# Kernel tuning notes

Measured on AMD Instinct MI355X. Metric: run time of the kernel, lower is better.

Reference implementation:

```python
import jax, jax.numpy as jnp
import numpy as np

N_GRAPH = 10000
IN_DIM = 256
HID = 256
N_NODES = 16
FEAT_DIM = 64
N_EDGES = 5
TAU = 0.01


def _gat(x, src, dst, W, al, ar, R, b, H, D, N):
    # DGL GATConv: fc -> per-head attention logits -> edge softmax over dst -> aggregate, residual fc, bias
    h = (x @ W).reshape(N, H, D)                      # [N,H,D]
    el = jnp.sum(h * al[None], -1)                    # [N,H]
    er = jnp.sum(h * ar[None], -1)                    # [N,H]
    e = jax.nn.leaky_relu(el[src] + er[dst], 0.2)     # [E,H]
    m = jax.ops.segment_max(e, dst, num_segments=N)
    ex = jnp.exp(e - m[dst])
    s = jax.ops.segment_sum(ex, dst, num_segments=N)
    alpha = ex / s[dst]                               # [E,H]
    out = jax.ops.segment_sum(alpha[:, :, None] * h[src], dst, num_segments=N)  # [N,H,D]
    out = out + (x @ R).reshape(N, H, D) + b.reshape(1, H, D)
    return out.reshape(N, H * D)


def _masked_softmax(vec, mask, eps=1e-8):
    m = mask.astype(vec.dtype)
    _vec = vec * m - 10000.0 * (1.0 - m)
    vmax = jnp.max(_vec, axis=-1, keepdims=True)
    exps = jnp.exp((vec - vmax) * m) * m
    return exps / (jnp.sum(exps, -1, keepdims=True) + eps)


def _sample_edges(probs, target_idx):
    n, T = probs.shape
    mask = jnp.arange(T) == target_idx                # [T] bool, one-hot of target
    edges = [jnp.full((n,), target_idx, dtype=jnp.int32)]
    key = jax.random.key(42)
    for i in range(N_EDGES - 1):
        p = _masked_softmax(probs, jnp.logical_not(mask))
        idx = jax.random.categorical(jax.random.fold_in(key, i),
                                     jnp.log(jnp.maximum(p, 1e-30)), axis=-1)  # [n]
        mask = jnp.logical_or(jax.nn.one_hot(idx, T, dtype=bool), mask)
        edges.append(idx.astype(jnp.int32))
    return jnp.stack(edges, axis=-1)                  # [n, N_EDGES]


def _forward(feat, W1a, al1a, ar1a, R1a, b1a, W1e, al1e, ar1e, R1e, b1e,
             W2a, al2a, ar2a, R2a, b2a, W2e, al2e, ar2e, R2e, b2e,
             Wt, bt, Wo, bo, src, dst, target_idx):
    N = feat.shape[0]
    tf = jax.nn.leaky_relu(feat[target_idx] @ Wt + bt, 0.01)            # [2*HID]
    a = _gat(feat, src, dst, W1a, al1a, ar1a, R1a, b1a, 4, HID // 4, N)  # [N,HID]
    e = _gat(feat, src, dst, W1e, al1e, ar1e, R1e, b1e, 4, HID // 4, N)  # [N,HID]
    a2 = jax.nn.leaky_relu(jnp.concatenate([a, e], -1) + tf, 0.01)       # [N,2*HID]
    e2 = jax.nn.leaky_relu(jnp.concatenate([e, a], -1) + tf, 0.01)
    a3 = _gat(a2, src, dst, W2a, al2a, ar2a, R2a, b2a, 4, N_NODES * FEAT_DIM // 4, N)  # [N, n_nodes*feat_dim]
    e3 = _gat(e2, src, dst, W2e, al2e, ar2e, R2e, b2e, 1, N_NODES, N)                  # [N, n_nodes]
    attr = a3.reshape(N, N_NODES, FEAT_DIM).mean(0)                     # [n_nodes, feat_dim]
    node_attr = jax.nn.leaky_relu(attr, 0.01) @ Wo + bo                 # [n_nodes, input_dim]
    probs = jax.nn.softmax(e3.T, axis=-1)                               # [n_nodes, N]
    return node_attr, probs


def setup_inputs() -> dict:
    key = jax.random.key(0)
    ks = jax.random.split(key, 32)
    N, IN, H = N_GRAPH, IN_DIM, 4
    E0 = 80000
    feat = jax.random.normal(ks[0], (N, IN), jnp.float32)
    loop = jnp.arange(N, dtype=jnp.int32)
    src = jnp.concatenate([jax.random.randint(ks[1], (E0,), 0, N, jnp.int32), loop])
    dst = jnp.concatenate([jax.random.randint(ks[2], (E0,), 0, N, jnp.int32), loop])

    def p(k, shape, fan):
        return jax.random.normal(k, shape, jnp.float32) * (1.0 / np.sqrt(fan))

    D1 = HID // 4
    D2a = N_NODES * FEAT_DIM // 4
    O2a = N_NODES * FEAT_DIM
    inp = dict(feat=feat, src=src, dst=dst, target_idx=7)
    # layer-1 attr / edge GATs
    inp.update(W1a=p(ks[3], (IN, HID), IN), al1a=p(ks[4], (H, D1), D1), ar1a=p(ks[5], (H, D1), D1),
               R1a=p(ks[6], (IN, HID), IN), b1a=p(ks[7], (HID,), HID))
    inp.update(W1e=p(ks[8], (IN, HID), IN), al1e=p(ks[9], (H, D1), D1), ar1e=p(ks[10], (H, D1), D1),
               R1e=p(ks[11], (IN, HID), IN), b1e=p(ks[12], (HID,), HID))
    # layer-2 attr GAT (4 heads) and edge GAT (1 head)
    inp.update(W2a=p(ks[13], (2 * HID, O2a), 2 * HID), al2a=p(ks[14], (H, D2a), D2a), ar2a=p(ks[15], (H, D2a), D2a),
               R2a=p(ks[16], (2 * HID, O2a), 2 * HID), b2a=p(ks[17], (O2a,), O2a))
    inp.update(W2e=p(ks[18], (2 * HID, N_NODES), 2 * HID), al2e=p(ks[19], (1, N_NODES), N_NODES),
               ar2e=p(ks[20], (1, N_NODES), N_NODES), R2e=p(ks[21], (2 * HID, N_NODES), 2 * HID),
               b2e=p(ks[22], (N_NODES,), N_NODES))
    # target feat layer and attr output layer
    inp.update(Wt=p(ks[23], (IN, 2 * HID), IN), bt=p(ks[24], (2 * HID,), 2 * HID),
               Wo=p(ks[25], (FEAT_DIM, IN), FEAT_DIM), bo=p(ks[26], (IN,), IN))
    return inp


def reference(feat, W1a, al1a, ar1a, R1a, b1a, W1e, al1e, ar1e, R1e, b1e,
              W2a, al2a, ar2a, R2a, b2a, W2e, al2e, ar2e, R2e, b2e,
              Wt, bt, Wo, bo, src, dst, target_idx):
    node_attr, probs = _forward(feat, W1a, al1a, ar1a, R1a, b1a, W1e, al1e, ar1e, R1e, b1e,
                                W2a, al2a, ar2a, R2a, b2a, W2e, al2e, ar2e, R2e, b2e,
                                Wt, bt, Wo, bo, src, dst, target_idx)
    node_edges = _sample_edges(probs, target_idx)
    # (node_attr, attr_sample_weights, node_edges, normalized_edge_sample_weights)
    return node_attr, node_attr, node_edges, probs
```

## Files before the change

kernel.cpp:

```cpp
#include <hip/hip_runtime.h>
#include <hip/hip_bf16.h>

#define NGR 10000
typedef unsigned int u32;
typedef __attribute__((ext_vector_type(8))) short short8;
typedef __attribute__((ext_vector_type(4))) float f32x4;

__device__ __forceinline__ void threefry(u32 k0, u32 k1, u32 c0, u32 c1, u32& o0, u32& o1) {
    u32 ks2 = k0 ^ k1 ^ 0x1BD11BDAu;
    u32 x0 = c0 + k0, x1 = c1 + k1;
#define TF_R(r) { x0 += x1; x1 = (x1 << r) | (x1 >> (32 - r)); x1 ^= x0; }
    TF_R(13) TF_R(15) TF_R(26) TF_R(6)
    x0 += k1; x1 += ks2 + 1u;
    TF_R(17) TF_R(29) TF_R(16) TF_R(24)
    x0 += ks2; x1 += k0 + 2u;
    TF_R(13) TF_R(15) TF_R(26) TF_R(6)
    x0 += k0; x1 += k1 + 3u;
    TF_R(17) TF_R(29) TF_R(16) TF_R(24)
    x0 += k1; x1 += ks2 + 4u;
    TF_R(13) TF_R(15) TF_R(26) TF_R(6)
    x0 += ks2; x1 += k0 + 5u;
#undef TF_R
    o0 = x0; o1 = x1;
}

__global__ void k_deg(const int* __restrict__ dst, int* __restrict__ deg, int E) {
    int i = blockIdx.x * blockDim.x + threadIdx.x;
    if (i < E) atomicAdd(&deg[dst[i]], 1);
}
__global__ void k_scan(const int* __restrict__ deg, int* __restrict__ rowptr, int n) {
    __shared__ int sums[256];
    __shared__ int excl[257];
    const int T = 256;
    int t = threadIdx.x;
    int per = (n + T - 1) / T;
    int lo = t * per, hi = min(lo + per, n);
    int s = 0;
    for (int i = lo; i < hi; ++i) s += deg[i];
    sums[t] = s;
    __syncthreads();
    if (t == 0) { int run = 0; for (int i = 0; i < T; ++i) { excl[i] = run; run += sums[i]; } excl[T] = run; }
    __syncthreads();
    int run = excl[t];
    for (int i = lo; i < hi; ++i) { rowptr[i] = run; run += deg[i]; }
    if (t == 0) rowptr[n] = excl[T];
}
__global__ void k_scatter(const int* __restrict__ dst, const int* __restrict__ rowptr,
                          int* __restrict__ cursor, int* __restrict__ colidx, int E) {
    int i = blockIdx.x * blockDim.x + threadIdx.x;
    if (i >= E) return;
    int d = dst[i];
    int pos = atomicAdd(&cursor[d], 1);
    colidx[rowptr[d] + pos] = i;
}

#define TINYF 1.17549435e-38f
__global__ __launch_bounds__(256) void k_prep(
    const float* __restrict__ feat, const int* __restrict__ tptr,
    const float* __restrict__ Wt, const float* __restrict__ bt,
    const float* __restrict__ W1a, const float* __restrict__ W1e,
    const float* __restrict__ R1a, const float* __restrict__ R1e,
    const float* __restrict__ b1a, const float* __restrict__ b1e,
    const float* __restrict__ W2a, const float* __restrict__ al2a, const float* __restrict__ ar2a,
    unsigned short* __restrict__ feathi, unsigned short* __restrict__ featlo,
    unsigned short* __restrict__ WThi, unsigned short* __restrict__ WTlo,
    float* __restrict__ tf, float* __restrict__ gum, float* __restrict__ wal,
    float* __restrict__ packb, float* __restrict__ zreg)
{
    __shared__ float sh[32 * 33];
    int b = blockIdx.x, tid = threadIdx.x;
    if (b < 2500) {
        int idx = b * 256 + tid;
        float4 v = ((const float4*)feat)[idx];
        ushort4 h, l;
        __hip_bfloat16 bb; float r;
        bb = __float2bfloat16(v.x); h.x = *(unsigned short*)&bb; r = v.x - __bfloat162float(bb);
        bb = __float2bfloat16(r);   l.x = *(unsigned short*)&bb;
        bb = __float2bfloat16(v.y); h.y = *(unsigned short*)&bb; r = v.y - __bfloat162float(bb);
        bb = __float2bfloat16(r);   l.y = *(unsigned short*)&bb;
        bb = __float2bfloat16(v.z); h.z = *(unsigned short*)&bb; r = v.z - __bfloat162float(bb);
        bb = __float2bfloat16(r);   l.z = *(unsigned short*)&bb;
        bb = __float2bfloat16(v.w); h.w = *(unsigned short*)&bb; r = v.w - __bfloat162float(bb);
        bb = __float2bfloat16(r);   l.w = *(unsigned short*)&bb;
        ((ushort4*)feathi)[idx] = h;
        ((ushort4*)featlo)[idx] = l;
        return;
    }
    b -= 2500;
    if (b < 256) {
        int bx = b >> 3, by = b & 7;
        int tx = tid & 31, ty = tid >> 5;
#pragma unroll
        for (int i = ty; i < 32; i += 8) {
            int k = by * 32 + i, c = bx * 32 + tx;
            float v;
            if (c < 256) v = W1a[k * 256 + c];
            else if (c < 512) v = W1e[k * 256 + c - 256];
            else if (c < 768) v = R1a[k * 256 + c - 512];
            else v = R1e[k * 256 + c - 768];
            sh[i * 33 + tx] = v;
        }
        __syncthreads();
#pragma unroll
        for (int i = ty; i < 32; i += 8) {
            float x = sh[tx * 33 + i];
            __hip_bfloat16 bh = __float2bfloat16(x);
            float r = x - __bfloat162float(bh);
            __hip_bfloat16 bl = __float2bfloat16(r);
            WThi[(size_t)(bx * 32 + i) * 256 + by * 32 + tx] = *(unsigned short*)&bh;
            WTlo[(size_t)(bx * 32 + i) * 256 + by * 32 + tx] = *(unsigned short*)&bl;
        }
        return;
    }
    b -= 256;
    if (b < 8) {
        float* frow = sh;
        float* red = sh + 256;
        int t = *tptr;
        frow[tid] = feat[t * 256 + tid];
        __syncthreads();
        int j = b * 64 + (tid & 63);
        int ks = (tid >> 6) * 64;
        float s = 0.f;
#pragma unroll 16
        for (int k = ks; k < ks + 64; ++k) s = fmaf(frow[k], Wt[(size_t)k * 512 + j], s);
        red[tid] = s;
        __syncthreads();
        if (tid < 64) {
            float v = red[tid] + red[tid + 64] + red[tid + 128] + red[tid + 192] + bt[j];
            tf[j] = v >= 0.f ? v : 0.01f * v;
        }
        return;
    }
    b -= 8;
    if (b < 2500) {
        int idx = b * 256 + tid;
        int it = idx / (16 * NGR);
        int f = idx - it * (16 * NGR);
        u32 fk0, fk1, o0, o1;
        threefry(0u, 42u, 0u, (u32)it, fk0, fk1);
        threefry(fk0, fk1, 0u, (u32)f, o0, o1);
        u32 bits = o0 ^ o1;
        float fl = __uint_as_float((bits >> 9) | 0x3F800000u) - 1.0f;
        float u = fmaxf(TINYF, fl + TINYF);
        gum[idx] = -logf(-logf(u));
        return;
    }
    b -= 2500;
    if (b < 16) {
        int o = b * 256 + tid;
        int k = o >> 3, q = o & 7, sel = q >> 2, hh = q & 3;
        const float* av = (sel ? ar2a : al2a) + hh * 256;
        const float* wr = W2a + (size_t)k * 1024 + hh * 256;
        float s = 0.f;
        for (int d = 0; d < 256; ++d) s = fmaf(wr[d], av[d], s);
        wal[k * 8 + q] = s;
        return;
    }
    b -= 16;
    if (b < 235) {
        int idx = b * 256 + tid;
        if (idx < NGR * 6) zreg[idx] = 0.f;
        return;
    }
    b -= 235;
    {
        int c = b * 256 + tid;
        packb[c] = (c < 512) ? 0.f : ((c < 768) ? b1a[c - 512] : b1e[c - 768]);
    }
}

__global__ __launch_bounds__(256) void gemm_bf16x3(
    const unsigned short* __restrict__ Ahi, const unsigned short* __restrict__ Alo,
    const unsigned short* __restrict__ Bhi, const unsigned short* __restrict__ Blo,
    float* __restrict__ C, const float* __restrict__ bias, int M)
{
    constexpr int K = 256;
    __shared__ unsigned short AsH[2][128 * 32];
    __shared__ unsigned short AsL[2][128 * 32];
    __shared__ unsigned short BsH[2][128 * 32];
    __shared__ unsigned short BsL[2][128 * 32];
    const int tid = threadIdx.x;
    const int lane = tid & 63;
    const int w = tid >> 6, wr = w >> 1, wc = w & 1;
    const int bm = blockIdx.y * 128, bn = blockIdx.x * 128;
    const int fr = lane & 15, fq = lane >> 4;
    const int srow = tid >> 2;
    const int sbyte = (tid & 3) * 16;
    f32x4 acc[4][4] = {};

    auto stage = [&](int b, int k0) {
        const char* pA[2] = {(const char*)Ahi, (const char*)Alo};
        const char* pB[2] = {(const char*)Bhi, (const char*)Blo};
        char* dA[2] = {(char*)AsH[b], (char*)AsL[b]};
        char* dB[2] = {(char*)BsH[b], (char*)BsL[b]};
#pragma unroll
        for (int q = 0; q < 2; ++q) {
            const char* ga0 = pA[q] + ((size_t)(bm + srow) * K + k0) * 2 + sbyte;
            const char* ga1 = pA[q] + ((size_t)(bm + 64 + srow) * K + k0) * 2 + sbyte;
            const char* gb0 = pB[q] + ((size_t)(bn + srow) * K + k0) * 2 + sbyte;
            const char* gb1 = pB[q] + ((size_t)(bn + 64 + srow) * K + k0) * 2 + sbyte;
            __builtin_amdgcn_global_load_lds((const __attribute__((address_space(1))) void*)ga0,
                (__attribute__((address_space(3))) void*)(dA[q] + tid * 16), 16, 0, 0);
            __builtin_amdgcn_global_load_lds((const __attribute__((address_space(1))) void*)ga1,
                (__attribute__((address_space(3))) void*)(dA[q] + 4096 + tid * 16), 16, 0, 0);
            __builtin_amdgcn_global_load_lds((const __attribute__((address_space(1))) void*)gb0,
                (__attribute__((address_space(3))) void*)(dB[q] + tid * 16), 16, 0, 0);
            __builtin_amdgcn_global_load_lds((const __attribute__((address_space(1))) void*)gb1,
                (__attribute__((address_space(3))) void*)(dB[q] + 4096 + tid * 16), 16, 0, 0);
        }
    };

    stage(0, 0);
    __syncthreads();
    int buf = 0;
    for (int t = 0; t < 8; ++t) {
        if (t < 7) stage(buf ^ 1, (t + 1) * 32);
        const char* ah = (const char*)AsH[buf];
        const char* al = (const char*)AsL[buf];
        const char* bh = (const char*)BsH[buf];
        const char* bl = (const char*)BsL[buf];
        short8 afh[4], afl[4], bfh[4], bfl[4];
#pragma unroll
        for (int m = 0; m < 4; ++m) {
            int o = (wr * 64 + m * 16 + fr) * 64 + fq * 16;
            afh[m] = *(const short8*)(ah + o);
            afl[m] = *(const short8*)(al + o);
        }
#pragma unroll
        for (int n = 0; n < 4; ++n) {
            int o = (wc * 64 + n * 16 + fr) * 64 + fq * 16;
            bfh[n] = *(const short8*)(bh + o);
            bfl[n] = *(const short8*)(bl + o);
        }
#pragma unroll
        for (int m = 0; m < 4; ++m)
#pragma unroll
            for (int n = 0; n < 4; ++n) {
                acc[m][n] = __builtin_amdgcn_mfma_f32_16x16x32_bf16(afl[m], bfh[n], acc[m][n], 0, 0, 0);
                acc[m][n] = __builtin_amdgcn_mfma_f32_16x16x32_bf16(afh[m], bfl[n], acc[m][n], 0, 0, 0);
                acc[m][n] = __builtin_amdgcn_mfma_f32_16x16x32_bf16(afh[m], bfh[n], acc[m][n], 0, 0, 0);
            }
        __syncthreads();
        buf ^= 1;
    }
#pragma unroll
    for (int m = 0; m < 4; ++m) {
#pragma unroll
        for (int i = 0; i < 4; ++i) {
            int row = bm + wr * 64 + m * 16 + fq * 4 + i;
            if (row >= M) continue;
#pragma unroll
            for (int n = 0; n < 4; ++n) {
                int col = bn + wc * 64 + n * 16 + fr;
                C[(size_t)row * 1024 + col] = acc[m][n][i] + bias[col];
            }
        }
    }
}

__global__ void k_el_er_l1(const float* __restrict__ h,
                           const float* __restrict__ al1a, const float* __restrict__ ar1a,
                           const float* __restrict__ al1e, const float* __restrict__ ar1e,
                           float* __restrict__ el, float* __restrict__ er, int N)
{
    int idx = blockIdx.x * blockDim.x + threadIdx.x;
    if (idx >= N * 8) return;
    int n = idx >> 3, sub = idx & 7;
    int role = sub >> 2, hh = sub & 3;
    const float* hp = h + (size_t)n * 1024 + role * 256 + hh * 64;
    const float* alp = (role ? al1e : al1a) + hh * 64;
    const float* arp = (role ? ar1e : ar1a) + hh * 64;
    float sl = 0.f, sr = 0.f;
    for (int d = 0; d < 64; d += 4) {
        float4 v = *(const float4*)(hp + d);
        float4 a4 = *(const float4*)(alp + d);
        float4 r4 = *(const float4*)(arp + d);
        sl = fmaf(v.x, a4.x, sl); sl = fmaf(v.y, a4.y, sl); sl = fmaf(v.z, a4.z, sl); sl = fmaf(v.w, a4.w, sl);
        sr = fmaf(v.x, r4.x, sr); sr = fmaf(v.y, r4.y, sr); sr = fmaf(v.z, r4.z, sr); sr = fmaf(v.w, r4.w, sr);
    }
    el[n * 8 + sub] = sl;
    er[n * 8 + sub] = sr;
}

__global__ void k_softmax_csr(const float* __restrict__ el, const float* __restrict__ er,
                              const int* __restrict__ rowptr, const int* __restrict__ colidx,
                              const int* __restrict__ src,
                              float* __restrict__ ee, int H, int hshift, int total)
{
    int idx = blockIdx.x * blockDim.x + threadIdx.x;
    if (idx >= total) return;
    int n = idx >> hshift, hh = idx & (H - 1);
    float ern = er[n * H + hh];
    int i0 = rowptr[n], i1 = rowptr[n + 1];
    float mx = -INFINITY;
    for (int i = i0; i < i1; ++i) {
        float v = el[src[colidx[i]] * H + hh] + ern;
        v = v >= 0.f ? v : 0.2f * v;
        mx = fmaxf(mx, v);
    }
    float s = 0.f;
    for (int i = i0; i < i1; ++i) {
        int e = colidx[i];
        float v = el[src[e] * H + hh] + ern;
        v = v >= 0.f ? v : 0.2f * v;
        float ex = expf(v - mx);
        ee[(size_t)e * H + hh] = ex;
        s += ex;
    }
    for (int i = i0; i < i1; ++i) {
        int e = colidx[i];
        ee[(size_t)e * H + hh] /= s;
    }
}

__global__ void k_agg_a2e2(const float* __restrict__ alpha,
                           const int* __restrict__ rowptr, const int* __restrict__ colidx,
                           const int* __restrict__ src,
                           const float* __restrict__ regionA, const float* __restrict__ tf,
                           float* __restrict__ a2e2, int total)
{
    int idx = blockIdx.x * blockDim.x + threadIdx.x;
    if (idx >= total) return;
    int n = idx >> 7, c4 = idx & 127;
    int hh = c4 >> 4;
    const float4* h4 = (const float4*)regionA;
    float4 acc = h4[(size_t)n * 256 + 128 + c4];
    int i1 = rowptr[n + 1];
    for (int i = rowptr[n]; i < i1; ++i) {
        int e = colidx[i];
        float a = alpha[(size_t)e * 8 + hh];
        float4 hv = h4[(size_t)src[e] * 256 + c4];
        acc.x = fmaf(a, hv.x, acc.x); acc.y = fmaf(a, hv.y, acc.y);
        acc.z = fmaf(a, hv.z, acc.z); acc.w = fmaf(a, hv.w, acc.w);
    }
    int c = c4 << 2;
    int cc = (c + 256) & 511;
    float4 ta = *(const float4*)(tf + c);
    float4 te = *(const float4*)(tf + cc);
    float4 xa, xe;
    xa.x = acc.x + ta.x; xa.y = acc.y + ta.y; xa.z = acc.z + ta.z; xa.w = acc.w + ta.w;
    xe.x = acc.x + te.x; xe.y = acc.y + te.y; xe.z = acc.z + te.z; xe.w = acc.w + te.w;
    xa.x = xa.x >= 0.f ? xa.x : 0.01f * xa.x;
    xa.y = xa.y >= 0.f ? xa.y : 0.01f * xa.y;
    xa.z = xa.z >= 0.f ? xa.z : 0.01f * xa.z;
    xa.w = xa.w >= 0.f ? xa.w : 0.01f * xa.w;
    xe.x = xe.x >= 0.f ? xe.x : 0.01f * xe.x;
    xe.y = xe.y >= 0.f ? xe.y : 0.01f * xe.y;
    xe.z = xe.z >= 0.f ? xe.z : 0.01f * xe.z;
    xe.w = xe.w >= 0.f ? xe.w : 0.01f * xe.w;
    *(float4*)(a2e2 + (size_t)n * 1024 + c) = xa;
    *(float4*)(a2e2 + (size_t)n * 1024 + 512 + cc) = xe;
}

__global__ __launch_bounds__(256) void k_node_linear(
    const float* __restrict__ a2e2,
    const float* __restrict__ We, const float* __restrict__ Re, const float* __restrict__ be,
    const float* __restrict__ wal,
    const float* __restrict__ al2e, const float* __restrict__ ar2e,
    float* __restrict__ h2e, float* __restrict__ e3,
    float* __restrict__ el2e, float* __restrict__ er2e,
    float* __restrict__ el2a, float* __restrict__ er2a)
{
    __shared__ float As[8 * 1024];
    __shared__ float red[2048];
    __shared__ float hl[8][16];
    int tid = threadIdx.x;
    int m0 = blockIdx.x * 8;
    for (int i = tid; i < 8 * 256; i += 256) {
        int row = i >> 8, c4 = (i & 255) << 2;
        *(float4*)(As + row * 1024 + c4) = *(const float4*)(a2e2 + (size_t)(m0 + row) * 1024 + c4);
    }
    __syncthreads();
    {
        int j = tid & 31, ks = tid >> 5;
        const float* B = (j < 16) ? We : Re;
        int jj = j & 15;
        float acc[8] = {};
        int k0 = ks * 64;
        for (int kk = 0; kk < 64; kk += 4) {
            int k = k0 + kk;
            float b0 = B[(k + 0) * 16 + jj];
            float b1 = B[(k + 1) * 16 + jj];
            float b2 = B[(k + 2) * 16 + jj];
            float b3 = B[(k + 3) * 16 + jj];
#pragma unroll
            for (int r = 0; r < 8; ++r) {
                float4 a = *(const float4*)(As + r * 1024 + 512 + k);
                acc[r] = fmaf(a.x, b0, acc[r]);
                acc[r] = fmaf(a.y, b1, acc[r]);
                acc[r] = fmaf(a.z, b2, acc[r]);
                acc[r] = fmaf(a.w, b3, acc[r]);
            }
        }
#pragma unroll
        for (int r = 0; r < 8; ++r) red[(r * 32 + j) * 8 + ks] = acc[r];
    }
    __syncthreads();
    {
        int r = tid >> 5, jo = tid & 31;
        const float* rp = red + (r * 32 + jo) * 8;
        float acc = ((rp[0] + rp[1]) + (rp[2] + rp[3])) + ((rp[4] + rp[5]) + (rp[6] + rp[7]));
        int m = m0 + r, jj = jo & 15;
        if (jo < 16) { h2e[(size_t)m * 16 + jj] = acc; hl[r][jj] = acc; }
        else         e3[(size_t)m * 16 + jj] = acc + be[jj];
    }
    __syncthreads();
    {
        int q = tid & 7, ks2 = tid >> 3;
        float acc[8] = {};
        int k0 = ks2 * 16;
        for (int kk = 0; kk < 16; ++kk) {
            int k = k0 + kk;
            float b = wal[k * 8 + q];
#pragma unroll
            for (int r = 0; r < 8; ++r)
                acc[r] = fmaf(As[r * 1024 + k], b, acc[r]);
        }
#pragma unroll
        for (int r = 0; r < 8; ++r) red[(r * 8 + q) * 32 + ks2] = acc[r];
    }
    __syncthreads();
    if (tid < 64) {
        const float* rp = red + tid * 32;
        float acc = 0.f;
#pragma unroll
        for (int g = 0; g < 32; ++g) acc += rp[g];
        int r = tid >> 3, q = tid & 7;
        int m = m0 + r;
        if (q < 4) el2a[m * 4 + q] = acc;
        else       er2a[m * 4 + (q - 4)] = acc;
    }
    if (tid >= 64 && tid < 72) {
        int rr = tid - 64;
        float sl = 0.f, sr = 0.f;
        const float* hp = hl[rr];
        for (int d = 0; d < 16; ++d) { float v = hp[d]; sl = fmaf(v, al2e[d], sl); sr = fmaf(v, ar2e[d], sr); }
        el2e[m0 + rr] = sl;
        er2e[m0 + rr] = sr;
    }
}

__global__ void k_sm_l2(const float* __restrict__ el2a, const float* __restrict__ er2a,
                        const float* __restrict__ el2e, const float* __restrict__ er2e,
                        const int* __restrict__ rowptr, const int* __restrict__ colidx,
                        const int* __restrict__ src,
                        const float* __restrict__ h2e,
                        float* __restrict__ walpha, float* __restrict__ e3, int N)
{
    int idx = blockIdx.x * blockDim.x + threadIdx.x;
    if (idx < N * 4) {
        int n = idx >> 2, hh = idx & 3;
        float ern = er2a[n * 4 + hh];
        int i0 = rowptr[n], i1 = rowptr[n + 1];
        float mx = -INFINITY;
        for (int i = i0; i < i1; ++i) {
            float v = el2a[src[colidx[i]] * 4 + hh] + ern;
            v = v >= 0.f ? v : 0.2f * v;
            mx = fmaxf(mx, v);
        }
        float s = 0.f;
        for (int i = i0; i < i1; ++i) {
            float v = el2a[src[colidx[i]] * 4 + hh] + ern;
            v = v >= 0.f ? v : 0.2f * v;
            s += expf(v - mx);
        }
        for (int i = i0; i < i1; ++i) {
            int e = colidx[i];
            int sn = src[e];
            float v = el2a[sn * 4 + hh] + ern;
            v = v >= 0.f ? v : 0.2f * v;
            float alpha = expf(v - mx) / s;
            atomicAdd(&walpha[sn * 4 + hh], alpha);
        }
        return;
    }
    int n = idx - N * 4;
    if (n >= N) return;
    float ern = er2e[n];
    int i0 = rowptr[n], i1 = rowptr[n + 1];
    float mx = -INFINITY;
    for (int i = i0; i < i1; ++i) {
        float v = el2e[src[colidx[i]]] + ern;
        v = v >= 0.f ? v : 0.2f * v;
        mx = fmaxf(mx, v);
    }
    float s = 0.f;
    for (int i = i0; i < i1; ++i) {
        float v = el2e[src[colidx[i]]] + ern;
        v = v >= 0.f ? v : 0.2f * v;
        s += expf(v - mx);
    }
    float4* e34 = (float4*)(e3 + (size_t)n * 16);
    float4 a0 = e34[0], a1 = e34[1], a2 = e34[2], a3 = e34[3];
    for (int i = i0; i < i1; ++i) {
        int e = colidx[i];
        int sn = src[e];
        float v = el2e[sn] + ern;
        v = v >= 0.f ? v : 0.2f * v;
        float al = expf(v - mx) / s;
        const float4* hp = (const float4*)(h2e + (size_t)sn * 16);
        float4 h0 = hp[0], h1 = hp[1], h2 = hp[2], h3 = hp[3];
        a0.x = fmaf(al, h0.x, a0.x); a0.y = fmaf(al, h0.y, a0.y); a0.z = fmaf(al, h0.z, a0.z); a0.w = fmaf(al, h0.w, a0.w);
        a1.x = fmaf(al, h1.x, a1.x); a1.y = fmaf(al, h1.y, a1.y); a1.z = fmaf(al, h1.z, a1.z); a1.w = fmaf(al, h1.w, a1.w);
        a2.x = fmaf(al, h2.x, a2.x); a2.y = fmaf(al, h2.y, a2.y); a2.z = fmaf(al, h2.z, a2.z); a2.w = fmaf(al, h2.w, a2.w);
        a3.x = fmaf(al, h3.x, a3.x); a3.y = fmaf(al, h3.y, a3.y); a3.z = fmaf(al, h3.z, a3.z); a3.w = fmaf(al, h3.w, a3.w);
    }
    e34[0] = a0; e34[1] = a1; e34[2] = a2; e34[3] = a3;
}

__global__ __launch_bounds__(256) void k_pwa(const float* __restrict__ a2e2,
                                             const float* __restrict__ walpha,
                                             float* __restrict__ pwa)
{
    int b = blockIdx.x, t = threadIdx.x;
    float acc[5][2] = {};
    int n0 = b * 80, n1 = min(n0 + 80, NGR);
    for (int n = n0; n < n1; ++n) {
        const float* row = a2e2 + (size_t)n * 1024;
        const float* wa = walpha + n * 4;
        float w0 = wa[0], w1 = wa[1], w2 = wa[2], w3 = wa[3];
        float x0 = row[t], x1 = row[t + 256];
        acc[0][0] = fmaf(w0, x0, acc[0][0]); acc[0][1] = fmaf(w0, x1, acc[0][1]);
        acc[1][0] = fmaf(w1, x0, acc[1][0]); acc[1][1] = fmaf(w1, x1, acc[1][1]);
        acc[2][0] = fmaf(w2, x0, acc[2][0]); acc[2][1] = fmaf(w2, x1, acc[2][1]);
        acc[3][0] = fmaf(w3, x0, acc[3][0]); acc[3][1] = fmaf(w3, x1, acc[3][1]);
        acc[4][0] += x0; acc[4][1] += x1;
    }
#pragma unroll
    for (int q = 0; q < 5; ++q) {
        pwa[(size_t)b * 2560 + q * 512 + t] = acc[q][0];
        pwa[(size_t)b * 2560 + q * 512 + t + 256] = acc[q][1];
    }
}
__global__ void k_pwa_fin(const float* __restrict__ pwa, float* __restrict__ waw)
{
    int idx = blockIdx.x * blockDim.x + threadIdx.x;
    if (idx >= 2560) return;
    float s = 0.f;
    for (int b = 0; b < 125; ++b) s += pwa[(size_t)b * 2560 + idx];
    waw[idx] = s;
}

__global__ __launch_bounds__(256) void k_gemv3(const float* __restrict__ waw,
                                               const float* __restrict__ W2a, const float* __restrict__ R2a,
                                               const float* __restrict__ b2a,
                                               float* __restrict__ attrL)
{
    __shared__ float red[256];
    int b = blockIdx.x, t = threadIdx.x;
    int c = b * 16 + (t & 15);
    int hh = (b * 16) >> 8;
    int ks = (t >> 4) * 32;
    const float* wh = waw + hh * 512;
    const float* w4 = waw + 4 * 512;
    float s = 0.f;
#pragma unroll 8
    for (int k = ks; k < ks + 32; ++k) {
        s = fmaf(wh[k], W2a[(size_t)k * 1024 + c], s);
        s = fmaf(w4[k], R2a[(size_t)k * 1024 + c], s);
    }
    red[t] = s;
    __syncthreads();
    if (t < 16) {
        float v = 0.f;
#pragma unroll
        for (int g = 0; g < 16; ++g) v += red[t + g * 16];
        v = v / (float)NGR + b2a[b * 16 + t];
        attrL[b * 16 + t] = v >= 0.f ? v : 0.01f * v;
    }
}

__global__ __launch_bounds__(256) void k_nattr2(const float* __restrict__ attrL,
                                                const float* __restrict__ Wo, const float* __restrict__ bo,
                                                float* __restrict__ out)
{
    __shared__ float al[64];
    int i = blockIdx.x, t = threadIdx.x;
    if (t < 64) al[t] = attrL[i * 64 + t];
    __syncthreads();
    float acc = 0.f;
#pragma unroll 8
    for (int d = 0; d < 64; ++d) acc = fmaf(al[d], Wo[d * 256 + t], acc);
    acc += bo[t];
    out[i * 256 + t] = acc;
    out[4096 + i * 256 + t] = acc;
}

__global__ __launch_bounds__(256) void k_e3stats(const float* __restrict__ e3,
                                                 float* __restrict__ pm, float* __restrict__ ps)
{
    __shared__ float lds[4000];
    __shared__ float redm[16][16];
    __shared__ float reds[16][16];
    __shared__ float cm[16];
    int b = blockIdx.x, tid = threadIdx.x;
    int base = b * 250 * 16;
    for (int i = tid; i < 4000; i += 256) lds[i] = e3[base + i];
    __syncthreads();
    int c = tid & 15, g = tid >> 4;
    float mx = -INFINITY;
    for (int q = g; q < 250; q += 16) mx = fmaxf(mx, lds[q * 16 + c]);
    redm[c][g] = mx;
    __syncthreads();
    if (tid < 16) {
        float m = redm[tid][0];
        for (int q = 1; q < 16; ++q) m = fmaxf(m, redm[tid][q]);
        cm[tid] = m;
    }
    __syncthreads();
    float mb = cm[c];
    float s = 0.f;
    for (int q = g; q < 250; q += 16) s += expf(lds[q * 16 + c] - mb);
    reds[c][g] = s;
    __syncthreads();
    if (tid < 16) {
        float ss = 0.f;
        for (int q = 0; q < 16; ++q) ss += reds[tid][q];
        pm[b * 16 + tid] = cm[tid];
        ps[b * 16 + tid] = ss;
    }
}

__global__ __launch_bounds__(256) void k_top5(const float* __restrict__ e3, const float* __restrict__ gum,
                                              const float* __restrict__ pm, const float* __restrict__ ps,
                                              float* __restrict__ probs,
                                              float* __restrict__ t5v, int* __restrict__ t5i)
{
    __shared__ float wv[4];
    __shared__ int wi[4];
    int chunk = blockIdx.x, y = blockIdx.y;
    int it = y >> 4, r = y & 15;
    int tid = threadIdx.x, lane = tid & 63, wid = tid >> 6;
    float M = -INFINITY;
    for (int b = 0; b < 40; ++b) M = fmaxf(M, pm[b * 16 + r]);
    float S = 0.f;
    for (int b = 0; b < 40; ++b) S += ps[b * 16 + r] * expf(pm[b * 16 + r] - M);
    float mxr = M, ssr = S;
    const float* g = gum + (size_t)y * NGR;
    int jb = chunk * 1250;
    float sv[5]; int si[5];
#pragma unroll
    for (int q = 0; q < 5; ++q) {
        int o = q * 256 + tid;
        float s = -INFINITY; int idx = 0x7FFFFFFF;
        if (o < 1250) {
            int j = jb + o;
            float p = expf(e3[(size_t)j * 16 + r] - mxr) / ssr;
            if (it == 0) probs[(size_t)r * NGR + j] = p;
            s = g[j] + p;
            idx = j;
        }
        sv[q] = s; si[q] = idx;
    }
    int outb = (y * 8 + chunk) * 5;
    for (int round = 0; round < 5; ++round) {
        float best = sv[0]; int bi = si[0];
#pragma unroll
        for (int q = 1; q < 5; ++q)
            if (sv[q] > best || (sv[q] == best && si[q] < bi)) { best = sv[q]; bi = si[q]; }
#pragma unroll
        for (int o = 32; o > 0; o >>= 1) {
            float ov = __shfl_xor(best, o, 64); int oi = __shfl_xor(bi, o, 64);
            if (ov > best || (ov == best && oi < bi)) { best = ov; bi = oi; }
        }
        if (lane == 0) { wv[wid] = best; wi[wid] = bi; }
        __syncthreads();
        float gbv = wv[0]; int gbi = wi[0];
#pragma unroll
        for (int w2 = 1; w2 < 4; ++w2) {
            float ov = wv[w2]; int oi = wi[w2];
            if (ov > gbv || (ov == gbv && oi < gbi)) { gbv = ov; gbi = oi; }
        }
        if (tid == 0) { t5v[outb + round] = gbv; t5i[outb + round] = gbi; }
#pragma unroll
        for (int q = 0; q < 5; ++q) if (si[q] == gbi) { sv[q] = -INFINITY; si[q] = 0x7FFFFFFF; }
        __syncthreads();
    }
}

__global__ void k_select(const int* __restrict__ tptr, const float* __restrict__ t5v,
                         const int* __restrict__ t5i, float* __restrict__ out_edges)
{
    int r = threadIdx.x;
    if (r >= 16) return;
    int s0 = *tptr, s1 = -1, s2 = -1, s3 = -1;
    out_edges[r * 5] = (float)s0;
    for (int it = 0; it < 4; ++it) {
        float best = -INFINITY; int bi = 0x7FFFFFFF;
        int base = (it * 16 + r) * 40;
        for (int c = 0; c < 40; ++c) {
            int idx = t5i[base + c];
            if (idx == s0 || idx == s1 || idx == s2 || idx == s3) continue;
            float v = t5v[base + c];
            if (v > best || (v == best && idx < bi)) { best = v; bi = idx; }
        }
        if (it == 0) s1 = bi; else if (it == 1) s2 = bi; else if (it == 2) s3 = bi;
        out_edges[r * 5 + it + 1] = (float)bi;
    }
}

extern "C" void kernel_launch(void* const* d_in, const int* in_sizes, int n_in,
                              void* d_out, int out_size, void* d_ws, size_t ws_size,
                              hipStream_t stream)
{
    const float* feat = (const float*)d_in[0];
    const int* src = (const int*)d_in[1];
    const int* dst = (const int*)d_in[2];
    const int* tptr = (const int*)d_in[3];
    const float* W1a = (const float*)d_in[4];  const float* al1a = (const float*)d_in[5];
    const float* ar1a = (const float*)d_in[6]; const float* R1a = (const float*)d_in[7];
    const float* b1a = (const float*)d_in[8];
    const float* W1e = (const float*)d_in[9];  const float* al1e = (const float*)d_in[10];
    const float* ar1e = (const float*)d_in[11]; const float* R1e = (const float*)d_in[12];
    const float* b1e = (const float*)d_in[13];
    const float* W2a = (const float*)d_in[14]; const float* al2a = (const float*)d_in[15];
    const float* ar2a = (const float*)d_in[16]; const float* R2a = (const float*)d_in[17];
    const float* b2a = (const float*)d_in[18];
    const float* W2e = (const float*)d_in[19]; const float* al2e = (const float*)d_in[20];
    const float* ar2e = (const float*)d_in[21]; const float* R2e = (const float*)d_in[22];
    const float* b2e = (const float*)d_in[23];
    const float* Wt = (const float*)d_in[24];  const float* bt = (const float*)d_in[25];
    const float* Wo = (const float*)d_in[26];  const float* bo = (const float*)d_in[27];
    const int E = in_sizes[1];
    const int N = NGR;

    float* ws = (float*)d_ws;
    float* regionA = ws;
    size_t off = (size_t)N * 1024;
    auto alloc = [&](size_t n) { float* p = ws + off; off += (n + 3) & ~(size_t)3; return p; };
    float* a2e2 = alloc((size_t)N * 1024);
    float* tf   = alloc(512);
    float* el1  = alloc((size_t)N * 8);
    float* er1  = alloc((size_t)N * 8);
    float* el2a = alloc((size_t)N * 4);
    float* er2a = alloc((size_t)N * 4);
    float* el2e = alloc(N);
    float* er2e = alloc(N);
    float* h2e  = alloc((size_t)N * 16);
    float* e3   = alloc((size_t)N * 16);
    float* ee1  = alloc((size_t)E * 8);
    float* packb = alloc(1024);
    float* gum   = alloc((size_t)4 * 16 * NGR);
    float* wal   = alloc(512 * 8);
    float* pwa   = alloc(125 * 2560);
    float* waw   = alloc(2560);
    float* attrL = alloc(1024);
    float* pm    = alloc(40 * 16);
    float* ps    = alloc(40 * 16);
    float* t5v   = alloc(64 * 40);
    int*   t5i   = (int*)alloc(64 * 40);
    unsigned short* feathi = (unsigned short*)alloc((size_t)10112 * 128);
    unsigned short* featlo = (unsigned short*)alloc((size_t)10112 * 128);
    unsigned short* WThi = (unsigned short*)alloc((size_t)1024 * 128);
    unsigned short* WTlo = (unsigned short*)alloc((size_t)1024 * 128);
    float* zstart = alloc((size_t)N * 6);
    float* walpha = zstart;
    int* deg    = (int*)(zstart + (size_t)N * 4);
    int* cursor = deg + N;
    int* rowptr = (int*)alloc(N + 1);
    int* colidx = (int*)alloc(E);

    float* out = (float*)d_out;
    float* out_edges = out + 8192;
    float* out_probs = out + 8272;

    dim3 blk(256);

    k_prep<<<5519, blk, 0, stream>>>(feat, tptr, Wt, bt, W1a, W1e, R1a, R1e, b1a, b1e,
                                     W2a, al2a, ar2a, feathi, featlo, WThi, WTlo,
                                     tf, gum, wal, packb, zstart);
    k_deg<<<(E + 255) / 256, blk, 0, stream>>>(dst, deg, E);
    k_scan<<<1, blk, 0, stream>>>(deg, rowptr, N);
    k_scatter<<<(E + 255) / 256, blk, 0, stream>>>(dst, rowptr, cursor, colidx, E);

    gemm_bf16x3<<<dim3(8, 79), blk, 0, stream>>>(feathi, featlo, WThi, WTlo, regionA, packb, N);
    k_el_er_l1<<<(N * 8 + 255) / 256, blk, 0, stream>>>(regionA, al1a, ar1a, al1e, ar1e, el1, er1, N);
    k_softmax_csr<<<(N * 8 + 255) / 256, blk, 0, stream>>>(el1, er1, rowptr, colidx, src, ee1, 8, 3, N * 8);
    k_agg_a2e2<<<(N * 128 + 255) / 256, blk, 0, stream>>>(ee1, rowptr, colidx, src,
                                                          regionA, tf, a2e2, N * 128);

    k_node_linear<<<N / 8, blk, 0, stream>>>(a2e2, W2e, R2e, b2e, wal, al2e, ar2e,
                                             h2e, e3, el2e, er2e, el2a, er2a);
    k_sm_l2<<<(N * 5 + 255) / 256, blk, 0, stream>>>(el2a, er2a, el2e, er2e,
                                                     rowptr, colidx, src, h2e, walpha, e3, N);

    k_pwa<<<125, blk, 0, stream>>>(a2e2, walpha, pwa);
    k_pwa_fin<<<10, blk, 0, stream>>>(pwa, waw);
    k_gemv3<<<64, blk, 0, stream>>>(waw, W2a, R2a, b2a, attrL);
    k_nattr2<<<16, blk, 0, stream>>>(attrL, Wo, bo, out);

    k_e3stats<<<40, blk, 0, stream>>>(e3, pm, ps);
    k_top5<<<dim3(8, 64), blk, 0, stream>>>(e3, gum, pm, ps, out_probs, t5v, t5i);
    k_select<<<1, 64, 0, stream>>>(tptr, t5v, t5i, out_edges);
}
```

Before: 322.2 us.

## Store pre-activation aggregate once and recompute target-feature activation in consumers

The aggregation kernel now writes only the raw 512-wide accumulated GAT output per node instead of two 512-wide activated copies (with the target feature added). The add of the target feature and the leaky-ReLU are recomputed on the fly in the node-linear and pwa kernels. This halves the intermediate buffer written and re-read, cutting memory traffic at the cost of some redundant ALU work. The neighbour loop is also unrolled by two so more gathers are in flight.

```diff
diff --git a/kernel.cpp b/kernel.cpp
--- a/kernel.cpp
+++ b/kernel.cpp
@@ -314,11 +314,11 @@
     }
 }
 
-__global__ void k_agg_a2e2(const float* __restrict__ alpha,
-                           const int* __restrict__ rowptr, const int* __restrict__ colidx,
-                           const int* __restrict__ src,
-                           const float* __restrict__ regionA, const float* __restrict__ tf,
-                           float* __restrict__ a2e2, int total)
+__global__ void k_agg_acc(const float* __restrict__ alpha,
+                          const int* __restrict__ rowptr, const int* __restrict__ colidx,
+                          const int* __restrict__ src,
+                          const float* __restrict__ regionA,
+                          float* __restrict__ accb, int total)
 {
     int idx = blockIdx.x * blockDim.x + threadIdx.x;
     if (idx >= total) return;
@@ -326,35 +326,31 @@
     int hh = c4 >> 4;
     const float4* h4 = (const float4*)regionA;
     float4 acc = h4[(size_t)n * 256 + 128 + c4];
-    int i1 = rowptr[n + 1];
-    for (int i = rowptr[n]; i < i1; ++i) {
-        int e = colidx[i];
-        float a = alpha[(size_t)e * 8 + hh];
-        float4 hv = h4[(size_t)src[e] * 256 + c4];
-        acc.x = fmaf(a, hv.x, acc.x); acc.y = fmaf(a, hv.y, acc.y);
-        acc.z = fmaf(a, hv.z, acc.z); acc.w = fmaf(a, hv.w, acc.w);
-    }
-    int c = c4 << 2;
-    int cc = (c + 256) & 511;
-    float4 ta = *(const float4*)(tf + c);
-    float4 te = *(const float4*)(tf + cc);
-    float4 xa, xe;
-    xa.x = acc.x + ta.x; xa.y = acc.y + ta.y; xa.z = acc.z + ta.z; xa.w = acc.w + ta.w;
-    xe.x = acc.x + te.x; xe.y = acc.y + te.y; xe.z = acc.z + te.z; xe.w = acc.w + te.w;
-    xa.x = xa.x >= 0.f ? xa.x : 0.01f * xa.x;
-    xa.y = xa.y >= 0.f ? xa.y : 0.01f * xa.y;
-    xa.z = xa.z >= 0.f ? xa.z : 0.01f * xa.z;
-    xa.w = xa.w >= 0.f ? xa.w : 0.01f * xa.w;
-    xe.x = xe.x >= 0.f ? xe.x : 0.01f * xe.x;
-    xe.y = xe.y >= 0.f ? xe.y : 0.01f * xe.y;
-    xe.z = xe.z >= 0.f ? xe.z : 0.01f * xe.z;
-    xe.w = xe.w >= 0.f ? xe.w : 0.01f * xe.w;
-    *(float4*)(a2e2 + (size_t)n * 1024 + c) = xa;
-    *(float4*)(a2e2 + (size_t)n * 1024 + 512 + cc) = xe;
+    int i = rowptr[n], i1 = rowptr[n + 1];
+    for (; i + 1 < i1; i += 2) {
+        int e0 = colidx[i], e1 = colidx[i + 1];
+        int s0 = src[e0], s1 = src[e1];
+        float a0 = alpha[(size_t)e0 * 8 + hh];
+        float a1 = alpha[(size_t)e1 * 8 + hh];
+        float4 h0 = h4[(size_t)s0 * 256 + c4];
+        float4 h1 = h4[(size_t)s1 * 256 + c4];
+        acc.x = fmaf(a0, h0.x, acc.x); acc.y = fmaf(a0, h0.y, acc.y);
+        acc.z = fmaf(a0, h0.z, acc.z); acc.w = fmaf(a0, h0.w, acc.w);
+        acc.x = fmaf(a1, h1.x, acc.x); acc.y = fmaf(a1, h1.y, acc.y);
+        acc.z = fmaf(a1, h1.z, acc.z); acc.w = fmaf(a1, h1.w, acc.w);
+    }
+    if (i < i1) {
+        int e0 = colidx[i];
+        float a0 = alpha[(size_t)e0 * 8 + hh];
+        float4 h0 = h4[(size_t)src[e0] * 256 + c4];
+        acc.x = fmaf(a0, h0.x, acc.x); acc.y = fmaf(a0, h0.y, acc.y);
+        acc.z = fmaf(a0, h0.z, acc.z); acc.w = fmaf(a0, h0.w, acc.w);
+    }
+    ((float4*)accb)[(size_t)n * 128 + c4] = acc;
 }
 
 __global__ __launch_bounds__(256) void k_node_linear(
-    const float* __restrict__ a2e2,
+    const float* __restrict__ accb, const float* __restrict__ tf,
     const float* __restrict__ We, const float* __restrict__ Re, const float* __restrict__ be,
     const float* __restrict__ wal,
     const float* __restrict__ al2e, const float* __restrict__ ar2e,
@@ -367,9 +363,25 @@
     __shared__ float hl[8][16];
     int tid = threadIdx.x;
     int m0 = blockIdx.x * 8;
-    for (int i = tid; i < 8 * 256; i += 256) {
-        int row = i >> 8, c4 = (i & 255) << 2;
-        *(float4*)(As + row * 1024 + c4) = *(const float4*)(a2e2 + (size_t)(m0 + row) * 1024 + c4);
+    for (int i = tid; i < 8 * 128; i += 256) {
+        int row = i >> 7, c = (i & 127) << 2;
+        float4 a = *(const float4*)(accb + (size_t)(m0 + row) * 512 + c);
+        int cc = (c + 256) & 511;
+        float4 ta = *(const float4*)(tf + c);
+        float4 te = *(const float4*)(tf + cc);
+        float4 xa, xe;
+        xa.x = a.x + ta.x; xa.y = a.y + ta.y; xa.z = a.z + ta.z; xa.w = a.w + ta.w;
+        xe.x = a.x + te.x; xe.y = a.y + te.y; xe.z = a.z + te.z; xe.w = a.w + te.w;
+        xa.x = xa.x >= 0.f ? xa.x : 0.01f * xa.x;
+        xa.y = xa.y >= 0.f ? xa.y : 0.01f * xa.y;
+        xa.z = xa.z >= 0.f ? xa.z : 0.01f * xa.z;
+        xa.w = xa.w >= 0.f ? xa.w : 0.01f * xa.w;
+        xe.x = xe.x >= 0.f ? xe.x : 0.01f * xe.x;
+        xe.y = xe.y >= 0.f ? xe.y : 0.01f * xe.y;
+        xe.z = xe.z >= 0.f ? xe.z : 0.01f * xe.z;
+        xe.w = xe.w >= 0.f ? xe.w : 0.01f * xe.w;
+        *(float4*)(As + row * 1024 + c) = xa;
+        *(float4*)(As + row * 1024 + 512 + cc) = xe;
     }
     __syncthreads();
     {
@@ -509,18 +521,21 @@
     e34[0] = a0; e34[1] = a1; e34[2] = a2; e34[3] = a3;
 }
 
-__global__ __launch_bounds__(256) void k_pwa(const float* __restrict__ a2e2,
+__global__ __launch_bounds__(256) void k_pwa(const float* __restrict__ accb,
+                                             const float* __restrict__ tf,
                                              const float* __restrict__ walpha,
                                              float* __restrict__ pwa)
 {
     int b = blockIdx.x, t = threadIdx.x;
+    float tf0 = tf[t], tf1 = tf[t + 256];
     float acc[5][2] = {};
     int n0 = b * 80, n1 = min(n0 + 80, NGR);
     for (int n = n0; n < n1; ++n) {
-        const float* row = a2e2 + (size_t)n * 1024;
+        const float* row = accb + (size_t)n * 512;
         const float* wa = walpha + n * 4;
         float w0 = wa[0], w1 = wa[1], w2 = wa[2], w3 = wa[3];
-        float x0 = row[t], x1 = row[t + 256];
+        float x0 = row[t] + tf0;       x0 = x0 >= 0.f ? x0 : 0.01f * x0;
+        float x1 = row[t + 256] + tf1; x1 = x1 >= 0.f ? x1 : 0.01f * x1;
         acc[0][0] = fmaf(w0, x0, acc[0][0]); acc[0][1] = fmaf(w0, x1, acc[0][1]);
         acc[1][0] = fmaf(w1, x0, acc[1][0]); acc[1][1] = fmaf(w1, x1, acc[1][1]);
         acc[2][0] = fmaf(w2, x0, acc[2][0]); acc[2][1] = fmaf(w2, x1, acc[2][1]);
@@ -729,7 +744,7 @@
     float* regionA = ws;
     size_t off = (size_t)N * 1024;
     auto alloc = [&](size_t n) { float* p = ws + off; off += (n + 3) & ~(size_t)3; return p; };
-    float* a2e2 = alloc((size_t)N * 1024);
+    float* accb = alloc((size_t)N * 512);
     float* tf   = alloc(512);
     float* el1  = alloc((size_t)N * 8);
     float* er1  = alloc((size_t)N * 8);
@@ -777,15 +792,15 @@
     gemm_bf16x3<<<dim3(8, 79), blk, 0, stream>>>(feathi, featlo, WThi, WTlo, regionA, packb, N);
     k_el_er_l1<<<(N * 8 + 255) / 256, blk, 0, stream>>>(regionA, al1a, ar1a, al1e, ar1e, el1, er1, N);
     k_softmax_csr<<<(N * 8 + 255) / 256, blk, 0, stream>>>(el1, er1, rowptr, colidx, src, ee1, 8, 3, N * 8);
-    k_agg_a2e2<<<(N * 128 + 255) / 256, blk, 0, stream>>>(ee1, rowptr, colidx, src,
-                                                          regionA, tf, a2e2, N * 128);
-
-    k_node_linear<<<N / 8, blk, 0, stream>>>(a2e2, W2e, R2e, b2e, wal, al2e, ar2e,
+    k_agg_acc<<<(N * 128 + 255) / 256, blk, 0, stream>>>(ee1, rowptr, colidx, src,
+                                                         regionA, accb, N * 128);
+
+    k_node_linear<<<N / 8, blk, 0, stream>>>(accb, tf, W2e, R2e, b2e, wal, al2e, ar2e,
                                              h2e, e3, el2e, er2e, el2a, er2a);
     k_sm_l2<<<(N * 5 + 255) / 256, blk, 0, stream>>>(el2a, er2a, el2e, er2e,
                                                      rowptr, colidx, src, h2e, walpha, e3, N);
 
-    k_pwa<<<125, blk, 0, stream>>>(a2e2, walpha, pwa);
+    k_pwa<<<125, blk, 0, stream>>>(accb, tf, walpha, pwa);
     k_pwa_fin<<<10, blk, 0, stream>>>(pwa, waw);
     k_gemv3<<<64, blk, 0, stream>>>(waw, W2a, R2a, b2a, attrL);
     k_nattr2<<<16, blk, 0, stream>>>(attrL, Wo, bo, out);
```

Result: faster. 314.2 us (-2.5%).
